# Optimization experiments

Hardware: AMD Instinct MI355X
Metric: run time of the kernel (lower is better)

The kernel has to match this reference:

```python
import jax, jax.numpy as jnp
import numpy as np

N_NODES = 10000
N_EDGES = 320000
DIM = 256
EDGE_DIM = 64
HEADS = 4
HEAD_DIM = DIM // HEADS
K_HOPS = 3
GAMMA = 0.5
FF_HIDDEN = 512


def setup_inputs() -> dict:
    key = jax.random.key(0)
    ks = jax.random.split(key, 8)
    x = jax.random.normal(ks[0], (N_NODES, DIM), dtype=jnp.float32)
    edge_index = jax.random.randint(ks[1], (2, N_EDGES), 0, N_NODES, dtype=jnp.int64)
    edge_attr = jax.random.normal(ks[2], (N_EDGES, EDGE_DIM), dtype=jnp.float32)
    W_x = jax.random.normal(ks[3], (DIM, DIM), dtype=jnp.float32) / np.sqrt(DIM)
    W_e = jax.random.normal(ks[4], (EDGE_DIM, DIM), dtype=jnp.float32) / np.sqrt(EDGE_DIM)
    att_a = jax.random.normal(ks[5], (HEADS, HEAD_DIM), dtype=jnp.float32) / np.sqrt(HEAD_DIM)
    W_ff1 = jax.random.normal(ks[6], (DIM, FF_HIDDEN), dtype=jnp.float32) / np.sqrt(DIM)
    W_ff2 = jax.random.normal(ks[7], (FF_HIDDEN, DIM), dtype=jnp.float32) / np.sqrt(FF_HIDDEN)
    return {"x": x, "edge_index": edge_index, "edge_attr": edge_attr,
            "W_x": W_x, "W_e": W_e, "att_a": att_a, "W_ff1": W_ff1, "W_ff2": W_ff2}


def reference(x, edge_index, edge_attr, W_x, W_e, att_a, W_ff1, W_ff2):
    N = x.shape[0]
    src, dst = edge_index[0], edge_index[1]

    h0 = x @ W_x                     # (N, H*D) linear node transform
    e = edge_attr @ W_e              # (E, H*D) linear edge transform
    deg = jax.ops.segment_sum(jnp.ones_like(src, dtype=x.dtype), dst,
                              num_segments=N)  # (N,)

    # K-hop propagation with graph elimination: remove gamma-weighted
    # backtracking contribution of the hop-(k-2) state.
    hops = [h0]
    h_prev2 = jnp.zeros_like(h0)
    h_prev1 = h0
    for _ in range(K_HOPS):
        m = jax.nn.relu(h_prev1[src] + e)                       # (E, H*D)
        agg = jax.ops.segment_sum(m, dst, num_segments=N)       # (N, H*D)
        h_k = agg - GAMMA * deg[:, None] * h_prev2
        hops.append(h_k)
        h_prev2, h_prev1 = h_prev1, h_k

    hs = jnp.stack(hops, 0).reshape(K_HOPS + 1, N, HEADS, HEAD_DIM)  # (K+1,N,H,D)

    # Per-head hop attention: query is the hop-0 (center) representation.
    q = hs[0]                                                        # (N,H,D)
    scores = jnp.einsum('hd,knhd->knh', att_a, jnp.tanh(hs + q[None]))
    alpha = jax.nn.softmax(scores, axis=0)                           # (K+1,N,H)
    out = jnp.einsum('knh,knhd->nhd', alpha, hs).reshape(N, DIM)     # concat heads

    # use_ffN: residual feed-forward
    out = out + jax.nn.relu(out @ W_ff1) @ W_ff2

    # wrapper: act (ReLU) + dropout(eval=identity) + residual
    out = jax.nn.relu(out)
    return x + out
```

## Files before the change

### kernel.cpp

```cpp
#include <hip/hip_runtime.h>
#include <hip/hip_bf16.h>

#define N_NODES   10000
#define N_EDGES   320000
#define DIM       256
#define EDGE_DIM  64
#define FF_HIDDEN 512
#define GAMMA     0.5f

typedef __attribute__((ext_vector_type(8))) short bf16x8;
typedef __attribute__((ext_vector_type(4))) float f32x4;

static __device__ __forceinline__ unsigned short f2b(float f)
{
    union { __hip_bfloat16 b; unsigned short u; } c;
    c.b = __float2bfloat16(f);
    return c.u;
}
static __device__ __forceinline__ float b2f(unsigned short u)
{
    union { unsigned u32; float f; } c;
    c.u32 = ((unsigned)u) << 16;
    return c.f;
}

static __device__ __forceinline__ bf16x8 load_a_frag(const float* __restrict__ p)
{
    const float4 f0 = *(const float4*)p;
    const float4 f1 = *(const float4*)(p + 4);
    bf16x8 r;
    r[0] = (short)f2b(f0.x); r[1] = (short)f2b(f0.y);
    r[2] = (short)f2b(f0.z); r[3] = (short)f2b(f0.w);
    r[4] = (short)f2b(f1.x); r[5] = (short)f2b(f1.y);
    r[6] = (short)f2b(f1.z); r[7] = (short)f2b(f1.w);
    return r;
}

__global__ __launch_bounds__(256) void detect_kernel(const unsigned* __restrict__ ei,
                                                     int* __restrict__ flag)
{
    __shared__ int bad;
    if (threadIdx.x == 0) bad = 0;
    __syncthreads();
    int b = 0;
    for (int i = threadIdx.x; i < 1024; i += 256)
        if (ei[2 * i + 1] != 0u) b = 1;
    if (b) atomicAdd(&bad, 1);
    __syncthreads();
    if (threadIdx.x == 0) *flag = (bad == 0) ? 1 : 0;
}

__global__ __launch_bounds__(256) void convert_kernel(const unsigned* __restrict__ ei,
                                                      const int* __restrict__ flag,
                                                      int* __restrict__ src, int* __restrict__ dst,
                                                      int* __restrict__ counts)
{
    const int i = blockIdx.x * 256 + threadIdx.x;
    if (i >= N_EDGES) return;
    const int f = *flag;
    int s, d;
    if (f) { s = (int)ei[2 * i]; d = (int)ei[2 * (N_EDGES + i)]; }
    else   { s = (int)ei[i];     d = (int)ei[N_EDGES + i]; }
    src[i] = s;
    dst[i] = d;
    atomicAdd(&counts[d], 1);
}

__global__ __launch_bounds__(256) void scan_kernel(const int* __restrict__ counts,
                                                   int* __restrict__ row_start)
{
    __shared__ int lds[256];
    const int t = threadIdx.x;
    int vals[40];
    int tot = 0;
    const int base = t * 40;
#pragma unroll
    for (int j = 0; j < 40; ++j) {
        const int idx = base + j;
        const int c = (idx < N_NODES) ? counts[idx] : 0;
        vals[j] = tot;
        tot += c;
    }
    lds[t] = tot;
    __syncthreads();
    for (int off = 1; off < 256; off <<= 1) {
        const int tmp = (t >= off) ? lds[t - off] : 0;
        __syncthreads();
        lds[t] += tmp;
        __syncthreads();
    }
    const int ebase = lds[t] - tot;
#pragma unroll
    for (int j = 0; j < 40; ++j) {
        const int idx = base + j;
        if (idx < N_NODES) row_start[idx] = ebase + vals[j];
    }
    if (t == 0) row_start[N_NODES] = N_EDGES;
}

__global__ __launch_bounds__(256) void fill_kernel(const int* __restrict__ src,
                                                   const int* __restrict__ dst,
                                                   const int* __restrict__ row_start,
                                                   int* __restrict__ fillc,
                                                   int* __restrict__ csr_eid,
                                                   int* __restrict__ csr_src)
{
    const int i = blockIdx.x * 256 + threadIdx.x;
    if (i >= N_EDGES) return;
    const int d = dst[i];
    const int pos = atomicAdd(&fillc[d], 1);
    const int slot = row_start[d] + pos;
    csr_eid[slot] = i;
    csr_src[slot] = src[i];
}

__global__ __launch_bounds__(256) void wconv_kernel(const float* __restrict__ W,
                                                    unsigned short* __restrict__ wT,
                                                    int K, int N)
{
    const int i = blockIdx.x * 256 + threadIdx.x;
    if (i >= K * N) return;
    const int k = i / N, n = i - k * N;
    wT[(size_t)n * K + k] = f2b(W[i]);
}

template <bool ABF16, int MODE>
__global__ __launch_bounds__(256) void wgemm(const void* __restrict__ Av,
                                             const unsigned short* __restrict__ wT,
                                             void* __restrict__ outv,
                                             int M, int K, int N,
                                             const unsigned short* __restrict__ epi_a,
                                             const float* __restrict__ epi_x)
{
    const int tid  = threadIdx.x;
    const int wave = tid >> 6;
    const int lane = tid & 63;
    const int l15  = lane & 15;
    const int l4   = lane >> 4;
    const int m0   = blockIdx.x * 64;
    const int n0   = blockIdx.y * 256 + wave * 64;

    f32x4 acc[4][4];
#pragma unroll
    for (int i = 0; i < 4; ++i)
#pragma unroll
        for (int j = 0; j < 4; ++j) acc[i][j] = f32x4{0.f, 0.f, 0.f, 0.f};

    int rowm[4];
#pragma unroll
    for (int i = 0; i < 4; ++i) rowm[i] = min(m0 + i * 16 + l15, M - 1);

    const int nk = K >> 6;
    for (int kt = 0; kt < nk; ++kt) {
        const int kb = kt * 64 + l4 * 8;
        bf16x8 bfr[2][4], afr[2][4];
#pragma unroll
        for (int ks = 0; ks < 2; ++ks)
#pragma unroll
            for (int j = 0; j < 4; ++j)
                bfr[ks][j] = *(const bf16x8*)(wT + (size_t)(n0 + j * 16 + l15) * K + kb + ks * 32);
#pragma unroll
        for (int ks = 0; ks < 2; ++ks)
#pragma unroll
            for (int i = 0; i < 4; ++i) {
                if (ABF16)
                    afr[ks][i] = *(const bf16x8*)((const unsigned short*)Av + (size_t)rowm[i] * K + kb + ks * 32);
                else
                    afr[ks][i] = load_a_frag((const float*)Av + (size_t)rowm[i] * K + kb + ks * 32);
            }
#pragma unroll
        for (int ks = 0; ks < 2; ++ks)
#pragma unroll
            for (int i = 0; i < 4; ++i)
#pragma unroll
                for (int j = 0; j < 4; ++j)
                    acc[i][j] = __builtin_amdgcn_mfma_f32_16x16x32_bf16(bfr[ks][j], afr[ks][i], acc[i][j], 0, 0, 0);
    }

#pragma unroll
    for (int i = 0; i < 4; ++i) {
        const int m = m0 + i * 16 + l15;
        if (m < M) {
#pragma unroll
            for (int j = 0; j < 4; ++j) {
                const size_t oi = (size_t)m * N + n0 + j * 16 + l4 * 4;
                if (MODE == 2) {
                    const ushort4 ea = *(const ushort4*)(epi_a + oi);
                    const float4  ex = *(const float4*)(epi_x + oi);
                    float4 v;
                    v.x = fmaxf(acc[i][j][0] + b2f(ea.x), 0.f) + ex.x;
                    v.y = fmaxf(acc[i][j][1] + b2f(ea.y), 0.f) + ex.y;
                    v.z = fmaxf(acc[i][j][2] + b2f(ea.z), 0.f) + ex.z;
                    v.w = fmaxf(acc[i][j][3] + b2f(ea.w), 0.f) + ex.w;
                    *(float4*)((float*)outv + oi) = v;
                } else {
                    float a0 = acc[i][j][0], a1 = acc[i][j][1];
                    float a2 = acc[i][j][2], a3 = acc[i][j][3];
                    if (MODE == 1) {
                        a0 = fmaxf(a0, 0.f); a1 = fmaxf(a1, 0.f);
                        a2 = fmaxf(a2, 0.f); a3 = fmaxf(a3, 0.f);
                    }
                    ushort4 u;
                    u.x = f2b(a0); u.y = f2b(a1); u.z = f2b(a2); u.w = f2b(a3);
                    *(ushort4*)((unsigned short*)outv + oi) = u;
                }
            }
        }
    }
}

__global__ __launch_bounds__(256) void egemm_kernel(const float* __restrict__ A,
                                                    const unsigned short* __restrict__ wT,
                                                    unsigned short* __restrict__ e_out,
                                                    const int* __restrict__ csr_eid)
{
    const int tid  = threadIdx.x;
    const int wave = tid >> 6;
    const int lane = tid & 63;
    const int l15  = lane & 15;
    const int l4   = lane >> 4;
    const int wc0  = wave * 64;
    const int m0   = blockIdx.x * 64;

    bf16x8 bfr[2][4];
#pragma unroll
    for (int ks = 0; ks < 2; ++ks)
#pragma unroll
        for (int j = 0; j < 4; ++j)
            bfr[ks][j] = *(const bf16x8*)(wT + (size_t)(wc0 + j * 16 + l15) * 64 + ks * 32 + l4 * 8);

    int eid[4];
#pragma unroll
    for (int i = 0; i < 4; ++i) eid[i] = csr_eid[m0 + i * 16 + l15];

    bf16x8 afr[2][4];
#pragma unroll
    for (int ks = 0; ks < 2; ++ks)
#pragma unroll
        for (int i = 0; i < 4; ++i)
            afr[ks][i] = load_a_frag(A + (size_t)eid[i] * 64 + ks * 32 + l4 * 8);

    f32x4 acc[4][4];
#pragma unroll
    for (int i = 0; i < 4; ++i)
#pragma unroll
        for (int j = 0; j < 4; ++j) acc[i][j] = f32x4{0.f, 0.f, 0.f, 0.f};
#pragma unroll
    for (int ks = 0; ks < 2; ++ks)
#pragma unroll
        for (int i = 0; i < 4; ++i)
#pragma unroll
            for (int j = 0; j < 4; ++j)
                acc[i][j] = __builtin_amdgcn_mfma_f32_16x16x32_bf16(bfr[ks][j], afr[ks][i], acc[i][j], 0, 0, 0);

#pragma unroll
    for (int i = 0; i < 4; ++i) {
#pragma unroll
        for (int j = 0; j < 4; ++j) {
            ushort4 u;
            u.x = f2b(acc[i][j][0]); u.y = f2b(acc[i][j][1]);
            u.z = f2b(acc[i][j][2]); u.w = f2b(acc[i][j][3]);
            *(ushort4*)(e_out + (size_t)(m0 + i * 16 + l15) * 256 + wc0 + j * 16 + l4 * 4) = u;
        }
    }
}

__global__ __launch_bounds__(256) void hop_kernel(const unsigned short* __restrict__ h_prev1,
                                                  const unsigned short* __restrict__ h_prev2,
                                                  const unsigned short* __restrict__ e,
                                                  const int* __restrict__ row_start,
                                                  const int* __restrict__ csr_src,
                                                  unsigned short* __restrict__ h_out)
{
    const int wave = threadIdx.x >> 6;
    const int lane = threadIdx.x & 63;
    const int n = blockIdx.x * 4 + wave;
    const int d4 = lane * 4;
    const int rb = row_start[n];
    const int re = row_start[n + 1];

    float4 acc = {0.f, 0.f, 0.f, 0.f};
    int s = rb;
    for (; s + 8 <= re; s += 8) {
        int idx[8];
        ushort4 ev[8], hv[8];
#pragma unroll
        for (int u = 0; u < 8; ++u) idx[u] = csr_src[s + u];
#pragma unroll
        for (int u = 0; u < 8; ++u) ev[u] = *(const ushort4*)(e + (size_t)(s + u) * DIM + d4);
#pragma unroll
        for (int u = 0; u < 8; ++u) hv[u] = *(const ushort4*)(h_prev1 + (size_t)idx[u] * DIM + d4);
#pragma unroll
        for (int u = 0; u < 8; ++u) {
            acc.x += fmaxf(b2f(hv[u].x) + b2f(ev[u].x), 0.f);
            acc.y += fmaxf(b2f(hv[u].y) + b2f(ev[u].y), 0.f);
            acc.z += fmaxf(b2f(hv[u].z) + b2f(ev[u].z), 0.f);
            acc.w += fmaxf(b2f(hv[u].w) + b2f(ev[u].w), 0.f);
        }
    }
    for (; s < re; ++s) {
        const int sr = csr_src[s];
        const ushort4 ev = *(const ushort4*)(e + (size_t)s * DIM + d4);
        const ushort4 hv = *(const ushort4*)(h_prev1 + (size_t)sr * DIM + d4);
        acc.x += fmaxf(b2f(hv.x) + b2f(ev.x), 0.f);
        acc.y += fmaxf(b2f(hv.y) + b2f(ev.y), 0.f);
        acc.z += fmaxf(b2f(hv.z) + b2f(ev.z), 0.f);
        acc.w += fmaxf(b2f(hv.w) + b2f(ev.w), 0.f);
    }
    if (h_prev2) {
        const float gd = GAMMA * (float)(re - rb);
        const ushort4 p2 = *(const ushort4*)(h_prev2 + (size_t)n * DIM + d4);
        acc.x -= gd * b2f(p2.x); acc.y -= gd * b2f(p2.y);
        acc.z -= gd * b2f(p2.z); acc.w -= gd * b2f(p2.w);
    }
    ushort4 o;
    o.x = f2b(acc.x); o.y = f2b(acc.y); o.z = f2b(acc.z); o.w = f2b(acc.w);
    *(ushort4*)(h_out + (size_t)n * DIM + d4) = o;
}

__global__ __launch_bounds__(256) void attn_kernel(const unsigned short* __restrict__ h0,
                                                   const unsigned short* __restrict__ h1,
                                                   const unsigned short* __restrict__ h2,
                                                   const unsigned short* __restrict__ h3,
                                                   const float* __restrict__ att_a,
                                                   unsigned short* __restrict__ out)
{
    const int n = blockIdx.x;
    const int t = threadIdx.x;
    const size_t i = (size_t)n * DIM + t;
    const float q = b2f(h0[i]);
    float hk[4];
    hk[0] = q; hk[1] = b2f(h1[i]); hk[2] = b2f(h2[i]); hk[3] = b2f(h3[i]);
    const float a = att_a[t];
    float sc[4];
#pragma unroll
    for (int k = 0; k < 4; ++k) {
        float v = tanhf(hk[k] + q) * a;
#pragma unroll
        for (int off = 32; off > 0; off >>= 1)
            v += __shfl_xor(v, off, 64);
        sc[k] = v;
    }
    const float mx = fmaxf(fmaxf(sc[0], sc[1]), fmaxf(sc[2], sc[3]));
    float ex[4], se = 0.f;
#pragma unroll
    for (int k = 0; k < 4; ++k) { ex[k] = __expf(sc[k] - mx); se += ex[k]; }
    const float inv = 1.f / se;
    float o = 0.f;
#pragma unroll
    for (int k = 0; k < 4; ++k) o += ex[k] * inv * hk[k];
    out[i] = f2b(o);
}

extern "C" void kernel_launch(void* const* d_in, const int* in_sizes, int n_in,
                              void* d_out, int out_size, void* d_ws, size_t ws_size,
                              hipStream_t stream)
{
    const float*    x         = (const float*)d_in[0];
    const unsigned* ei        = (const unsigned*)d_in[1];
    const float*    edge_attr = (const float*)d_in[2];
    const float*    W_x       = (const float*)d_in[3];
    const float*    W_e       = (const float*)d_in[4];
    const float*    att_a     = (const float*)d_in[5];
    const float*    W_ff1     = (const float*)d_in[6];
    const float*    W_ff2     = (const float*)d_in[7];

    char* ws = (char*)d_ws;
    size_t off = 0;
    auto alloc = [&](size_t bytes) -> void* {
        void* p = ws + off;
        off = (off + bytes + 255) & ~(size_t)255;
        return p;
    };
    int*   flag      = (int*)alloc(4);
    int*   src32     = (int*)alloc((size_t)N_EDGES * 4);
    int*   dst32     = (int*)alloc((size_t)N_EDGES * 4);
    int*   counts    = (int*)alloc((size_t)2 * N_NODES * 4);
    int*   fillc     = counts + N_NODES;
    int*   row_start = (int*)alloc((size_t)(N_NODES + 1) * 4);
    int*   csr_eid   = (int*)alloc((size_t)N_EDGES * 4);
    int*   csr_src   = (int*)alloc((size_t)N_EDGES * 4);
    unsigned short* h0b   = (unsigned short*)alloc((size_t)N_NODES * DIM * 2);
    unsigned short* h1b   = (unsigned short*)alloc((size_t)N_NODES * DIM * 2);
    unsigned short* h2b   = (unsigned short*)alloc((size_t)N_NODES * DIM * 2);
    unsigned short* h3b   = (unsigned short*)alloc((size_t)N_NODES * DIM * 2);
    unsigned short* e_bf  = (unsigned short*)alloc((size_t)N_EDGES * DIM * 2);
    unsigned short* attnb = (unsigned short*)alloc((size_t)N_NODES * DIM * 2);
    unsigned short* hidb  = (unsigned short*)alloc((size_t)N_NODES * FF_HIDDEN * 2);
    unsigned short* wxT   = (unsigned short*)alloc((size_t)DIM * DIM * 2);
    unsigned short* weT   = (unsigned short*)alloc((size_t)DIM * EDGE_DIM * 2);
    unsigned short* wff1T = (unsigned short*)alloc((size_t)FF_HIDDEN * DIM * 2);
    unsigned short* wff2T = (unsigned short*)alloc((size_t)DIM * FF_HIDDEN * 2);
    if (off > ws_size) return;

    const int egrid = (N_EDGES + 255) / 256;

    hipMemsetAsync(counts, 0, (size_t)2 * N_NODES * 4, stream);
    detect_kernel<<<1, 256, 0, stream>>>(ei, flag);
    convert_kernel<<<egrid, 256, 0, stream>>>(ei, flag, src32, dst32, counts);
    scan_kernel<<<1, 256, 0, stream>>>(counts, row_start);
    fill_kernel<<<egrid, 256, 0, stream>>>(src32, dst32, row_start, fillc, csr_eid, csr_src);

    wconv_kernel<<<(DIM * DIM + 255) / 256, 256, 0, stream>>>(W_x, wxT, DIM, DIM);
    wconv_kernel<<<(EDGE_DIM * DIM + 255) / 256, 256, 0, stream>>>(W_e, weT, EDGE_DIM, DIM);
    wconv_kernel<<<(DIM * FF_HIDDEN + 255) / 256, 256, 0, stream>>>(W_ff1, wff1T, DIM, FF_HIDDEN);
    wconv_kernel<<<(FF_HIDDEN * DIM + 255) / 256, 256, 0, stream>>>(W_ff2, wff2T, FF_HIDDEN, DIM);

    wgemm<false, 0><<<dim3(157, 1), 256, 0, stream>>>(x, wxT, h0b,
        N_NODES, DIM, DIM, nullptr, nullptr);
    egemm_kernel<<<N_EDGES / 64, 256, 0, stream>>>(edge_attr, weT, e_bf, csr_eid);

    hop_kernel<<<N_NODES / 4, 256, 0, stream>>>(h0b, nullptr, e_bf, row_start, csr_src, h1b);
    hop_kernel<<<N_NODES / 4, 256, 0, stream>>>(h1b, h0b,     e_bf, row_start, csr_src, h2b);
    hop_kernel<<<N_NODES / 4, 256, 0, stream>>>(h2b, h1b,     e_bf, row_start, csr_src, h3b);

    attn_kernel<<<N_NODES, 256, 0, stream>>>(h0b, h1b, h2b, h3b, att_a, attnb);

    wgemm<true, 1><<<dim3(157, 2), 256, 0, stream>>>(attnb, wff1T, hidb,
        N_NODES, DIM, FF_HIDDEN, nullptr, nullptr);
    wgemm<true, 2><<<dim3(157, 1), 256, 0, stream>>>(hidb, wff2T, d_out,
        N_NODES, FF_HIDDEN, DIM, attnb, x);
}
```

Baseline: 395.1 us.

## Recompute edge transform inside each hop instead of materializing edge features

Drops the (E,256) bf16 edge-feature buffer. Each hop now runs a fused kernel that recomputes edge_attr@W_e with MFMA from a CSR-ordered bf16 copy of edge_attr, adds the gathered source state, applies ReLU, and reduces per-destination sums through LDS before atomically adding to an fp32 accumulator. A fixup kernel then applies the gamma-degree correction and converts back to bf16. This removes the large e write and three re-reads, at the cost of redoing the small GEMM each hop, fp32 atomics, memsets, and nondeterministic summation order.

```diff
diff --git a/kernel.cpp b/kernel.cpp
--- a/kernel.cpp
+++ b/kernel.cpp
@@ -7,6 +7,7 @@
 #define EDGE_DIM  64
 #define FF_HIDDEN 512
 #define GAMMA     0.5f
+#define LSTR      260
 
 typedef __attribute__((ext_vector_type(8))) short bf16x8;
 typedef __attribute__((ext_vector_type(4))) float f32x4;
@@ -103,7 +104,8 @@
                                                    const int* __restrict__ row_start,
                                                    int* __restrict__ fillc,
                                                    int* __restrict__ csr_eid,
-                                                   int* __restrict__ csr_src)
+                                                   int* __restrict__ csr_src,
+                                                   int* __restrict__ csr_dst)
 {
     const int i = blockIdx.x * 256 + threadIdx.x;
     if (i >= N_EDGES) return;
@@ -112,6 +114,7 @@
     const int slot = row_start[d] + pos;
     csr_eid[slot] = i;
     csr_src[slot] = src[i];
+    csr_dst[slot] = d;
 }
 
 __global__ __launch_bounds__(256) void wconv_kernel(const float* __restrict__ W,
@@ -122,6 +125,19 @@
     if (i >= K * N) return;
     const int k = i / N, n = i - k * N;
     wT[(size_t)n * K + k] = f2b(W[i]);
+}
+
+__global__ __launch_bounds__(256) void ea_conv(const float* __restrict__ ea,
+                                               const int* __restrict__ csr_eid,
+                                               unsigned short* __restrict__ out)
+{
+    const int slot = blockIdx.x * 16 + (threadIdx.x >> 4);
+    const int l = threadIdx.x & 15;
+    const int eid = csr_eid[slot];
+    const float4 f = *(const float4*)(ea + (size_t)eid * EDGE_DIM + l * 4);
+    ushort4 u;
+    u.x = f2b(f.x); u.y = f2b(f.y); u.z = f2b(f.z); u.w = f2b(f.w);
+    *(ushort4*)(out + (size_t)slot * EDGE_DIM + l * 4) = u;
 }
 
 template <bool ABF16, int MODE>
@@ -209,36 +225,43 @@
     }
 }
 
-__global__ __launch_bounds__(256) void egemm_kernel(const float* __restrict__ A,
-                                                    const unsigned short* __restrict__ wT,
-                                                    unsigned short* __restrict__ e_out,
-                                                    const int* __restrict__ csr_eid)
-{
+__global__ __launch_bounds__(256) void fused_hop(const unsigned short* __restrict__ h_prev1,
+                                                 const unsigned short* __restrict__ ea,
+                                                 const unsigned short* __restrict__ weT,
+                                                 const int* __restrict__ csr_src,
+                                                 const int* __restrict__ csr_dst,
+                                                 float* __restrict__ agg)
+{
+    __shared__ unsigned short val[64 * LSTR];
+    __shared__ int dst_l[64];
+
     const int tid  = threadIdx.x;
     const int wave = tid >> 6;
     const int lane = tid & 63;
     const int l15  = lane & 15;
     const int l4   = lane >> 4;
     const int wc0  = wave * 64;
-    const int m0   = blockIdx.x * 64;
+    const int s0   = blockIdx.x * 64;
+
+    if (tid < 64) dst_l[tid] = csr_dst[s0 + tid];
 
     bf16x8 bfr[2][4];
 #pragma unroll
     for (int ks = 0; ks < 2; ++ks)
 #pragma unroll
         for (int j = 0; j < 4; ++j)
-            bfr[ks][j] = *(const bf16x8*)(wT + (size_t)(wc0 + j * 16 + l15) * 64 + ks * 32 + l4 * 8);
-
-    int eid[4];
-#pragma unroll
-    for (int i = 0; i < 4; ++i) eid[i] = csr_eid[m0 + i * 16 + l15];
+            bfr[ks][j] = *(const bf16x8*)(weT + (size_t)(wc0 + j * 16 + l15) * 64 + ks * 32 + l4 * 8);
 
     bf16x8 afr[2][4];
 #pragma unroll
     for (int ks = 0; ks < 2; ++ks)
 #pragma unroll
         for (int i = 0; i < 4; ++i)
-            afr[ks][i] = load_a_frag(A + (size_t)eid[i] * 64 + ks * 32 + l4 * 8);
+            afr[ks][i] = *(const bf16x8*)(ea + (size_t)(s0 + i * 16 + l15) * 64 + ks * 32 + l4 * 8);
+
+    int srcs[4];
+#pragma unroll
+    for (int i = 0; i < 4; ++i) srcs[i] = csr_src[s0 + i * 16 + l15];
 
     f32x4 acc[4][4];
 #pragma unroll
@@ -255,66 +278,52 @@
 
 #pragma unroll
     for (int i = 0; i < 4; ++i) {
+        const unsigned short* hp = h_prev1 + (size_t)srcs[i] * DIM + wc0 + l4 * 4;
 #pragma unroll
         for (int j = 0; j < 4; ++j) {
+            const ushort4 hv = *(const ushort4*)(hp + j * 16);
             ushort4 u;
-            u.x = f2b(acc[i][j][0]); u.y = f2b(acc[i][j][1]);
-            u.z = f2b(acc[i][j][2]); u.w = f2b(acc[i][j][3]);
-            *(ushort4*)(e_out + (size_t)(m0 + i * 16 + l15) * 256 + wc0 + j * 16 + l4 * 4) = u;
+            u.x = f2b(fmaxf(acc[i][j][0] + b2f(hv.x), 0.f));
+            u.y = f2b(fmaxf(acc[i][j][1] + b2f(hv.y), 0.f));
+            u.z = f2b(fmaxf(acc[i][j][2] + b2f(hv.z), 0.f));
+            u.w = f2b(fmaxf(acc[i][j][3] + b2f(hv.w), 0.f));
+            *(ushort4*)(&val[(i * 16 + l15) * LSTR + wc0 + j * 16 + l4 * 4]) = u;
         }
     }
-}
-
-__global__ __launch_bounds__(256) void hop_kernel(const unsigned short* __restrict__ h_prev1,
-                                                  const unsigned short* __restrict__ h_prev2,
-                                                  const unsigned short* __restrict__ e,
-                                                  const int* __restrict__ row_start,
-                                                  const int* __restrict__ csr_src,
-                                                  unsigned short* __restrict__ h_out)
-{
-    const int wave = threadIdx.x >> 6;
-    const int lane = threadIdx.x & 63;
-    const int n = blockIdx.x * 4 + wave;
-    const int d4 = lane * 4;
-    const int rb = row_start[n];
-    const int re = row_start[n + 1];
-
-    float4 acc = {0.f, 0.f, 0.f, 0.f};
-    int s = rb;
-    for (; s + 8 <= re; s += 8) {
-        int idx[8];
-        ushort4 ev[8], hv[8];
-#pragma unroll
-        for (int u = 0; u < 8; ++u) idx[u] = csr_src[s + u];
-#pragma unroll
-        for (int u = 0; u < 8; ++u) ev[u] = *(const ushort4*)(e + (size_t)(s + u) * DIM + d4);
-#pragma unroll
-        for (int u = 0; u < 8; ++u) hv[u] = *(const ushort4*)(h_prev1 + (size_t)idx[u] * DIM + d4);
-#pragma unroll
-        for (int u = 0; u < 8; ++u) {
-            acc.x += fmaxf(b2f(hv[u].x) + b2f(ev[u].x), 0.f);
-            acc.y += fmaxf(b2f(hv[u].y) + b2f(ev[u].y), 0.f);
-            acc.z += fmaxf(b2f(hv[u].z) + b2f(ev[u].z), 0.f);
-            acc.w += fmaxf(b2f(hv[u].w) + b2f(ev[u].w), 0.f);
+    __syncthreads();
+
+    float sum = 0.f;
+    int cur = dst_l[0];
+    for (int s = 0; s < 64; ++s) {
+        const int nd = dst_l[s];
+        if (nd != cur) {
+            atomicAdd(&agg[(size_t)cur * DIM + tid], sum);
+            sum = 0.f;
+            cur = nd;
         }
-    }
-    for (; s < re; ++s) {
-        const int sr = csr_src[s];
-        const ushort4 ev = *(const ushort4*)(e + (size_t)s * DIM + d4);
-        const ushort4 hv = *(const ushort4*)(h_prev1 + (size_t)sr * DIM + d4);
-        acc.x += fmaxf(b2f(hv.x) + b2f(ev.x), 0.f);
-        acc.y += fmaxf(b2f(hv.y) + b2f(ev.y), 0.f);
-        acc.z += fmaxf(b2f(hv.z) + b2f(ev.z), 0.f);
-        acc.w += fmaxf(b2f(hv.w) + b2f(ev.w), 0.f);
-    }
+        sum += b2f(val[s * LSTR + tid]);
+    }
+    atomicAdd(&agg[(size_t)cur * DIM + tid], sum);
+}
+
+__global__ __launch_bounds__(256) void fixup_kernel(const float* __restrict__ agg,
+                                                    const unsigned short* __restrict__ h_prev2,
+                                                    const int* __restrict__ row_start,
+                                                    unsigned short* __restrict__ h_out)
+{
+    const int idx = blockIdx.x * 256 + threadIdx.x;
+    const int n  = idx >> 6;
+    const int d4 = (idx & 63) * 4;
+    const float4 a = *(const float4*)(agg + (size_t)n * DIM + d4);
+    float4 r = a;
     if (h_prev2) {
-        const float gd = GAMMA * (float)(re - rb);
+        const float gd = GAMMA * (float)(row_start[n + 1] - row_start[n]);
         const ushort4 p2 = *(const ushort4*)(h_prev2 + (size_t)n * DIM + d4);
-        acc.x -= gd * b2f(p2.x); acc.y -= gd * b2f(p2.y);
-        acc.z -= gd * b2f(p2.z); acc.w -= gd * b2f(p2.w);
+        r.x -= gd * b2f(p2.x); r.y -= gd * b2f(p2.y);
+        r.z -= gd * b2f(p2.z); r.w -= gd * b2f(p2.w);
     }
     ushort4 o;
-    o.x = f2b(acc.x); o.y = f2b(acc.y); o.z = f2b(acc.z); o.w = f2b(acc.w);
+    o.x = f2b(r.x); o.y = f2b(r.y); o.z = f2b(r.z); o.w = f2b(r.w);
     *(ushort4*)(h_out + (size_t)n * DIM + d4) = o;
 }
 
@@ -380,11 +389,13 @@
     int*   row_start = (int*)alloc((size_t)(N_NODES + 1) * 4);
     int*   csr_eid   = (int*)alloc((size_t)N_EDGES * 4);
     int*   csr_src   = (int*)alloc((size_t)N_EDGES * 4);
+    int*   csr_dst   = (int*)alloc((size_t)N_EDGES * 4);
+    unsigned short* ea_bf = (unsigned short*)alloc((size_t)N_EDGES * EDGE_DIM * 2);
+    float* agg       = (float*)alloc((size_t)N_NODES * DIM * 4);
     unsigned short* h0b   = (unsigned short*)alloc((size_t)N_NODES * DIM * 2);
     unsigned short* h1b   = (unsigned short*)alloc((size_t)N_NODES * DIM * 2);
     unsigned short* h2b   = (unsigned short*)alloc((size_t)N_NODES * DIM * 2);
     unsigned short* h3b   = (unsigned short*)alloc((size_t)N_NODES * DIM * 2);
-    unsigned short* e_bf  = (unsigned short*)alloc((size_t)N_EDGES * DIM * 2);
     unsigned short* attnb = (unsigned short*)alloc((size_t)N_NODES * DIM * 2);
     unsigned short* hidb  = (unsigned short*)alloc((size_t)N_NODES * FF_HIDDEN * 2);
     unsigned short* wxT   = (unsigned short*)alloc((size_t)DIM * DIM * 2);
@@ -399,20 +410,29 @@
     detect_kernel<<<1, 256, 0, stream>>>(ei, flag);
     convert_kernel<<<egrid, 256, 0, stream>>>(ei, flag, src32, dst32, counts);
     scan_kernel<<<1, 256, 0, stream>>>(counts, row_start);
-    fill_kernel<<<egrid, 256, 0, stream>>>(src32, dst32, row_start, fillc, csr_eid, csr_src);
+    fill_kernel<<<egrid, 256, 0, stream>>>(src32, dst32, row_start, fillc,
+                                           csr_eid, csr_src, csr_dst);
 
     wconv_kernel<<<(DIM * DIM + 255) / 256, 256, 0, stream>>>(W_x, wxT, DIM, DIM);
     wconv_kernel<<<(EDGE_DIM * DIM + 255) / 256, 256, 0, stream>>>(W_e, weT, EDGE_DIM, DIM);
     wconv_kernel<<<(DIM * FF_HIDDEN + 255) / 256, 256, 0, stream>>>(W_ff1, wff1T, DIM, FF_HIDDEN);
     wconv_kernel<<<(FF_HIDDEN * DIM + 255) / 256, 256, 0, stream>>>(W_ff2, wff2T, FF_HIDDEN, DIM);
 
+    ea_conv<<<N_EDGES / 16, 256, 0, stream>>>(edge_attr, csr_eid, ea_bf);
+
     wgemm<false, 0><<<dim3(157, 1), 256, 0, stream>>>(x, wxT, h0b,
         N_NODES, DIM, DIM, nullptr, nullptr);
-    egemm_kernel<<<N_EDGES / 64, 256, 0, stream>>>(edge_attr, weT, e_bf, csr_eid);
-
-    hop_kernel<<<N_NODES / 4, 256, 0, stream>>>(h0b, nullptr, e_bf, row_start, csr_src, h1b);
-    hop_kernel<<<N_NODES / 4, 256, 0, stream>>>(h1b, h0b,     e_bf, row_start, csr_src, h2b);
-    hop_kernel<<<N_NODES / 4, 256, 0, stream>>>(h2b, h1b,     e_bf, row_start, csr_src, h3b);
+
+    const size_t aggbytes = (size_t)N_NODES * DIM * 4;
+    hipMemsetAsync(agg, 0, aggbytes, stream);
+    fused_hop<<<N_EDGES / 64, 256, 0, stream>>>(h0b, ea_bf, weT, csr_src, csr_dst, agg);
+    fixup_kernel<<<N_NODES * 64 / 256, 256, 0, stream>>>(agg, nullptr, row_start, h1b);
+    hipMemsetAsync(agg, 0, aggbytes, stream);
+    fused_hop<<<N_EDGES / 64, 256, 0, stream>>>(h1b, ea_bf, weT, csr_src, csr_dst, agg);
+    fixup_kernel<<<N_NODES * 64 / 256, 256, 0, stream>>>(agg, h0b, row_start, h2b);
+    hipMemsetAsync(agg, 0, aggbytes, stream);
+    fused_hop<<<N_EDGES / 64, 256, 0, stream>>>(h2b, ea_bf, weT, csr_src, csr_dst, agg);
+    fixup_kernel<<<N_NODES * 64 / 256, 256, 0, stream>>>(agg, h1b, row_start, h3b);
 
     attn_kernel<<<N_NODES, 256, 0, stream>>>(h0b, h1b, h2b, h3b, att_a, attnb);
 
```

Result: slower. 461.4 us (+16.8%).
